# Kernel tuning notes

Measured on AMD Instinct MI355X. Metric: run time of the kernel, lower is better.

The kernel has to match this reference:

```python
import jax, jax.numpy as jnp
import numpy as np

N_NODES = 100000
N_EDGES = 1600000
D_IN = 128
D_HID = 128
D_OUT = 10
N_GRAPHS = 512


def setup_inputs() -> dict:
    key = jax.random.key(0)
    ks = jax.random.split(key, 12)
    x = jax.random.normal(ks[0], (N_NODES, D_IN), dtype=jnp.float32)
    edge_index = jax.random.randint(ks[1], (2, N_EDGES), 0, N_NODES, dtype=jnp.int64)
    batch = jnp.sort(jax.random.randint(ks[2], (N_NODES,), 0, N_GRAPHS, dtype=jnp.int64))
    s = 1.0 / np.sqrt(D_HID)
    W0 = jax.random.normal(ks[3], (D_HID, D_IN), dtype=jnp.float32) * s
    b0 = jax.random.normal(ks[4], (D_HID,), dtype=jnp.float32) * s
    W1 = jax.random.normal(ks[5], (D_HID, D_HID), dtype=jnp.float32) * s
    b1 = jax.random.normal(ks[6], (D_HID,), dtype=jnp.float32) * s
    W2 = jax.random.normal(ks[7], (D_HID, D_HID), dtype=jnp.float32) * s
    b2 = jax.random.normal(ks[8], (D_HID,), dtype=jnp.float32) * s
    Wg = jax.random.normal(ks[9], (D_OUT, D_HID), dtype=jnp.float32) * s
    bg = jax.random.normal(ks[10], (D_OUT,), dtype=jnp.float32) * s
    return {"x": x, "edge_index": edge_index, "batch": batch,
            "W0": W0, "b0": b0, "W1": W1, "b1": b1, "W2": W2, "b2": b2,
            "Wg": Wg, "bg": bg}


def _gin_conv(x, src, dst, W, b):
    # GINConv with eps=0: Linear(x + sum_{j in N(i)} x_j)
    agg = jax.ops.segment_sum(x[src], dst, num_segments=N_NODES)  # [N, d]
    return (x + agg) @ W.T + b


def reference(x, edge_index, batch, W0, b0, W1, b1, W2, b2, Wg, bg):
    src, dst = edge_index[0], edge_index[1]
    h = jax.nn.relu(_gin_conv(x, src, dst, W0, b0))
    h = jax.nn.relu(_gin_conv(h, src, dst, W1, b1))
    h = _gin_conv(h, src, dst, W2, b2)
    # global_mean_pool over graph ids
    sums = jax.ops.segment_sum(h, batch, num_segments=N_GRAPHS)            # [G, d]
    counts = jax.ops.segment_sum(jnp.ones((N_NODES,), h.dtype), batch, num_segments=N_GRAPHS)
    pooled = sums / jnp.maximum(counts, 1.0)[:, None]                       # [G, d]
    return pooled @ Wg.T + bg                                               # [G, out]
```

## Files before the change

### kernel.cpp

```cpp
#include <hip/hip_runtime.h>

#define N_NODES 100000
#define N_EDGES 1600000
#define N_GRAPHS 512
#define NBUCK 391
#define EPB 2048
#define NB_SCAT ((N_EDGES + EPB - 1) / EPB)
#define CAPB 4864
#define CONV_BLKS 6250

typedef _Float16 half8 __attribute__((ext_vector_type(8)));
typedef float floatx4 __attribute__((ext_vector_type(4)));

union U16 { uint4 u; half8 h; };

__global__ __launch_bounds__(256) void convert_pack(const float4* __restrict__ X4,
                                                    uint4* __restrict__ Xh,
                                                    const float* __restrict__ W0,
                                                    const float* __restrict__ W1,
                                                    const float* __restrict__ W2,
                                                    uint4* __restrict__ Bp,
                                                    int* __restrict__ gcur) {
    int bid = blockIdx.x, tid = threadIdx.x;
    if (bid < CONV_BLKS) {
        int t = bid * 256 + tid;
        float4 a = X4[t * 2], b = X4[t * 2 + 1];
        U16 o;
        o.h[0] = (_Float16)a.x; o.h[1] = (_Float16)a.y;
        o.h[2] = (_Float16)a.z; o.h[3] = (_Float16)a.w;
        o.h[4] = (_Float16)b.x; o.h[5] = (_Float16)b.y;
        o.h[6] = (_Float16)b.z; o.h[7] = (_Float16)b.w;
        Xh[t] = o.u;
    } else {
        int zi = (bid - CONV_BLKS) * 256 + tid;
        if (zi < NBUCK) gcur[zi] = 0;
        int slice = (bid - CONV_BLKS) * 4 + (tid >> 6);
        if (slice >= 96) return;
        int l = tid & 63;
        int layer = slice >> 5;
        int r = slice & 31;
        int c = r >> 3, f = r & 7;
        const float* W = (layer == 0) ? W0 : (layer == 1) ? W1 : W2;
        int col = f * 16 + (l & 15);
        int k0 = c * 32 + (l >> 4) * 8;
        U16 o;
        #pragma unroll
        for (int j = 0; j < 8; ++j) o.h[j] = (_Float16)W[col * 128 + k0 + j];
        Bp[layer * 2048 + (c * 8 + f) * 64 + l] = o.u;
    }
}

__global__ __launch_bounds__(256) void bucket_scatter(const int* __restrict__ src,
                                                      const int* __restrict__ dst,
                                                      int* __restrict__ gcur,
                                                      unsigned* __restrict__ pairs) {
    __shared__ int cnt[NBUCK];
    __shared__ int base[NBUCK];
    int tid = threadIdx.x;
    for (int i = tid; i < NBUCK; i += 256) cnt[i] = 0;
    __syncthreads();
    int e0 = blockIdx.x * EPB, e1 = min(e0 + EPB, N_EDGES);
    for (int e = e0 + tid; e < e1; e += 256) atomicAdd(&cnt[dst[e] >> 8], 1);
    __syncthreads();
    for (int i = tid; i < NBUCK; i += 256) {
        int v = cnt[i];
        base[i] = i * CAPB + (v ? atomicAdd(&gcur[i], v) : 0);
        cnt[i] = 0;
    }
    __syncthreads();
    for (int e = e0 + tid; e < e1; e += 256) {
        int d = dst[e], b = d >> 8;
        int r = atomicAdd(&cnt[b], 1);
        pairs[base[b] + r] = (unsigned)src[e] | ((unsigned)(d & 255) << 17);
    }
}

__global__ __launch_bounds__(256) void bucket_fine(const unsigned* __restrict__ pairs,
                                                   const int* __restrict__ gcur,
                                                   int* __restrict__ off,
                                                   int* __restrict__ srclist) {
    __shared__ int snap[NBUCK];
    __shared__ int ncnt[256];
    __shared__ int ws[4];
    int tid = threadIdx.x, b = blockIdx.x;
    int lane = tid & 63, w = tid >> 6;

    for (int i = tid; i < NBUCK; i += 256) snap[i] = gcur[i];
    ncnt[tid] = 0;
    __syncthreads();
    if (tid < 64) {
        int carry = 0;
        for (int base = 0; base < NBUCK; base += 64) {
            int i = base + tid;
            int v = (i < NBUCK) ? snap[i] : 0;
            int incl = v;
            #pragma unroll
            for (int s = 1; s < 64; s <<= 1) {
                int y = __shfl_up(incl, s, 64);
                if (tid >= s) incl += y;
            }
            if (i < NBUCK) snap[i] = carry + incl - v;
            carry += __shfl(incl, 63, 64);
        }
    }
    __syncthreads();
    int eLo = snap[b];
    int eNext = (b == NBUCK - 1) ? N_EDGES : snap[b + 1];
    int m = eNext - eLo;
    int sb = b * CAPB;
    if (b == 0 && tid == 0) off[N_NODES] = N_EDGES;
    __syncthreads();

    for (int t = tid; t < m; t += 256) {
        unsigned p = pairs[sb + t];
        atomicAdd(&ncnt[(p >> 17) & 255], 1);
    }
    __syncthreads();
    int v = ncnt[tid];
    int incl = v;
    #pragma unroll
    for (int s = 1; s < 64; s <<= 1) { int y = __shfl_up(incl, s, 64); if (lane >= s) incl += y; }
    if (lane == 63) ws[w] = incl;
    __syncthreads();
    if (tid < 4) {
        int t = ws[tid];
        #pragma unroll
        for (int s = 1; s < 4; s <<= 1) { int y = __shfl_up(t, s, 64); if (tid >= s) t += y; }
        ws[tid] = t;
    }
    __syncthreads();
    int excl = (w ? ws[w - 1] : 0) + incl - v;
    int n = (b << 8) + tid;
    if (n < N_NODES) off[n] = eLo + excl;
    __syncthreads();
    ncnt[tid] = excl;
    __syncthreads();
    for (int t = tid; t < m; t += 256) {
        unsigned p = pairs[sb + t];
        int r = atomicAdd(&ncnt[(p >> 17) & 255], 1);
        srclist[eLo + r] = (int)(p & 0x1FFFFu);
    }
}

__global__ __launch_bounds__(256) void gin_fused(const uint4* __restrict__ Xh,
                                                 const uint4* __restrict__ Bp,
                                                 const float* __restrict__ bias,
                                                 _Float16* __restrict__ H,
                                                 const int* __restrict__ off,
                                                 const int* __restrict__ srclist,
                                                 int doRelu) {
    __shared__ ushort lds[16 * 136];
    int tid = threadIdx.x;
    int n0 = blockIdx.x * 16;
    int r = tid >> 4;
    int c = tid & 15;
    int n = n0 + r;

    int j0 = off[n], j1 = off[n + 1];
    U16 acc; acc.u = Xh[(size_t)n * 16 + c];
    half8 a = acc.h;
    int j = j0;
    for (; j + 3 < j1; j += 4) {
        int s0 = srclist[j], s1 = srclist[j + 1], s2 = srclist[j + 2], s3 = srclist[j + 3];
        U16 v0, v1, v2, v3;
        v0.u = Xh[(size_t)s0 * 16 + c];
        v1.u = Xh[(size_t)s1 * 16 + c];
        v2.u = Xh[(size_t)s2 * 16 + c];
        v3.u = Xh[(size_t)s3 * 16 + c];
        a += v0.h; a += v1.h; a += v2.h; a += v3.h;
    }
    for (; j < j1; ++j) {
        U16 v; v.u = Xh[(size_t)srclist[j] * 16 + c];
        a += v.h;
    }
    U16 o; o.h = a;
    *(uint4*)&lds[r * 136 + c * 8] = o.u;
    __syncthreads();

    int wid = tid >> 6, lane = tid & 63;
    int lrow = lane & 15;
    int lk8 = (lane >> 4) * 8;

    floatx4 acc2[2];
    acc2[0] = (floatx4)0.f;
    acc2[1] = (floatx4)0.f;
    #pragma unroll
    for (int c4 = 0; c4 < 4; ++c4) {
        U16 af; af.u = *(const uint4*)&lds[lrow * 136 + c4 * 32 + lk8];
        #pragma unroll
        for (int q = 0; q < 2; ++q) {
            int f = wid * 2 + q;
            U16 b; b.u = Bp[(c4 * 8 + f) * 64 + lane];
            acc2[q] = __builtin_amdgcn_mfma_f32_16x16x32_f16(b.h, af.h, acc2[q], 0, 0, 0);
        }
    }

    int ncol = lane & 15;
    int rq = (lane >> 4) * 4;
    int node = n0 + ncol;
    #pragma unroll
    for (int q = 0; q < 2; ++q) {
        int f = wid * 2 + q;
        float4 bv = *(const float4*)(bias + f * 16 + rq);
        float o0 = acc2[q][0] + bv.x;
        float o1 = acc2[q][1] + bv.y;
        float o2 = acc2[q][2] + bv.z;
        float o3 = acc2[q][3] + bv.w;
        if (doRelu) {
            o0 = fmaxf(o0, 0.f); o1 = fmaxf(o1, 0.f);
            o2 = fmaxf(o2, 0.f); o3 = fmaxf(o3, 0.f);
        }
        ushort4 st;
        st.x = (unsigned short)__builtin_bit_cast(unsigned short, (_Float16)o0);
        st.y = (unsigned short)__builtin_bit_cast(unsigned short, (_Float16)o1);
        st.z = (unsigned short)__builtin_bit_cast(unsigned short, (_Float16)o2);
        st.w = (unsigned short)__builtin_bit_cast(unsigned short, (_Float16)o3);
        *(ushort4*)(H + (size_t)node * 128 + f * 16 + rq) = st;
    }
}

__device__ __forceinline__ int lower_bound_i(const int* a, int n, int val) {
    int lo = 0, hi = n;
    while (lo < hi) {
        int mid = (lo + hi) >> 1;
        if (a[mid] < val) lo = mid + 1; else hi = mid;
    }
    return lo;
}

__global__ __launch_bounds__(256) void pool_kernel(const uint4* __restrict__ Hh,
                                                   const int* __restrict__ batch,
                                                   const float* __restrict__ Wg,
                                                   const float* __restrict__ bg,
                                                   float* __restrict__ out) {
    __shared__ float p[16 * 128];
    __shared__ float pooled[128];
    int g = blockIdx.x, tid = threadIdx.x;
    int c = tid & 15, r = tid >> 4;
    int lo = lower_bound_i(batch, N_NODES, g);
    int hi = lower_bound_i(batch, N_NODES, g + 1);
    float acc[8] = {0, 0, 0, 0, 0, 0, 0, 0};
    for (int i = lo + r; i < hi; i += 16) {
        U16 v; v.u = Hh[(size_t)i * 16 + c];
        #pragma unroll
        for (int k = 0; k < 8; ++k) acc[k] += (float)v.h[k];
    }
    #pragma unroll
    for (int k = 0; k < 8; ++k) p[r * 128 + c * 8 + k] = acc[k];
    __syncthreads();
    if (tid < 128) {
        float s = 0.f;
        #pragma unroll
        for (int q = 0; q < 16; ++q) s += p[q * 128 + tid];
        pooled[tid] = s / fmaxf((float)(hi - lo), 1.0f);
    }
    __syncthreads();
    if (tid < 10) {
        float s = bg[tid];
        #pragma unroll 4
        for (int k = 0; k < 128; ++k) s += pooled[k] * Wg[tid * 128 + k];
        out[g * 10 + tid] = s;
    }
}

extern "C" void kernel_launch(void* const* d_in, const int* in_sizes, int n_in,
                              void* d_out, int out_size, void* d_ws, size_t ws_size,
                              hipStream_t stream) {
    const float* x   = (const float*)d_in[0];
    const int*   ei  = (const int*)d_in[1];
    const int*   bat = (const int*)d_in[2];
    const float* W0  = (const float*)d_in[3];
    const float* b0  = (const float*)d_in[4];
    const float* W1  = (const float*)d_in[5];
    const float* b1  = (const float*)d_in[6];
    const float* W2  = (const float*)d_in[7];
    const float* b2  = (const float*)d_in[8];
    const float* Wg  = (const float*)d_in[9];
    const float* bg  = (const float*)d_in[10];
    float* out = (float*)d_out;

    const int* src = ei;
    const int* dst = ei + N_EDGES;

    char* w = (char*)d_ws;
    unsigned* pairs = (unsigned*)(w);
    _Float16* P0    = (_Float16*)(w + 25600000);
    _Float16* P1    = (_Float16*)(w + 51200000);
    _Float16* P2    = (_Float16*)(w + 76800000);
    int*    srclist = (int*)(w + 102400000);
    int*    off     = (int*)(w + 108800000);
    uint4*  Bp      = (uint4*)(w + 109300000);
    int*    gcur    = (int*)(w + 109450000);

    convert_pack<<<CONV_BLKS + 24, 256, 0, stream>>>((const float4*)x, (uint4*)P0,
                                                     W0, W1, W2, Bp, gcur);
    bucket_scatter<<<NB_SCAT, 256, 0, stream>>>(src, dst, gcur, pairs);
    bucket_fine<<<NBUCK, 256, 0, stream>>>(pairs, gcur, off, srclist);

    int grid = N_NODES / 16;

    gin_fused<<<grid, 256, 0, stream>>>((const uint4*)P0, Bp, b0, P1, off, srclist, 1);
    gin_fused<<<grid, 256, 0, stream>>>((const uint4*)P1, Bp + 2048, b1, P2, off, srclist, 1);
    gin_fused<<<grid, 256, 0, stream>>>((const uint4*)P2, Bp + 4096, b2, P0, off, srclist, 0);

    pool_kernel<<<N_GRAPHS, 256, 0, stream>>>((const uint4*)P0, bat, Wg, bg, out);
}
```

Before: 282.6 us.

## Halve bucket width for edge sorting and process two node tiles per GIN block

The coarse edge bucketing now uses 128-node buckets (782 buckets) instead of 256-node buckets. This doubles the number of bucket_fine blocks, spreading that stage across more CUs, and shrinks the per-bucket scan to 128 entries. The GIN layer kernel now handles 32 nodes per block as two sequential 16-node gather+MFMA phases with separate LDS buffers, which halves the grid size. That fewer-but-longer-block scheme may lose latency hiding on the irregular gathers in exchange for a smaller launch and some amortised setup.

```diff
diff --git a/kernel.cpp b/kernel.cpp
--- a/kernel.cpp
+++ b/kernel.cpp
@@ -3,10 +3,10 @@
 #define N_NODES 100000
 #define N_EDGES 1600000
 #define N_GRAPHS 512
-#define NBUCK 391
+#define NBUCK 782
 #define EPB 2048
 #define NB_SCAT ((N_EDGES + EPB - 1) / EPB)
-#define CAPB 4864
+#define CAPB 2688
 #define CONV_BLKS 6250
 
 typedef _Float16 half8 __attribute__((ext_vector_type(8)));
@@ -60,7 +60,7 @@
     for (int i = tid; i < NBUCK; i += 256) cnt[i] = 0;
     __syncthreads();
     int e0 = blockIdx.x * EPB, e1 = min(e0 + EPB, N_EDGES);
-    for (int e = e0 + tid; e < e1; e += 256) atomicAdd(&cnt[dst[e] >> 8], 1);
+    for (int e = e0 + tid; e < e1; e += 256) atomicAdd(&cnt[dst[e] >> 7], 1);
     __syncthreads();
     for (int i = tid; i < NBUCK; i += 256) {
         int v = cnt[i];
@@ -69,9 +69,9 @@
     }
     __syncthreads();
     for (int e = e0 + tid; e < e1; e += 256) {
-        int d = dst[e], b = d >> 8;
+        int d = dst[e], b = d >> 7;
         int r = atomicAdd(&cnt[b], 1);
-        pairs[base[b] + r] = (unsigned)src[e] | ((unsigned)(d & 255) << 17);
+        pairs[base[b] + r] = (unsigned)src[e] | ((unsigned)(d & 127) << 17);
     }
 }
 
@@ -80,16 +80,16 @@
                                                    int* __restrict__ off,
                                                    int* __restrict__ srclist) {
     __shared__ int snap[NBUCK];
-    __shared__ int ncnt[256];
-    __shared__ int ws[4];
+    __shared__ int ncnt[128];
+    __shared__ int ws[2];
     int tid = threadIdx.x, b = blockIdx.x;
-    int lane = tid & 63, w = tid >> 6;
 
     for (int i = tid; i < NBUCK; i += 256) snap[i] = gcur[i];
-    ncnt[tid] = 0;
+    if (tid < 128) ncnt[tid] = 0;
     __syncthreads();
     if (tid < 64) {
         int carry = 0;
+        #pragma unroll 1
         for (int base = 0; base < NBUCK; base += 64) {
             int i = base + tid;
             int v = (i < NBUCK) ? snap[i] : 0;
@@ -113,49 +113,40 @@
 
     for (int t = tid; t < m; t += 256) {
         unsigned p = pairs[sb + t];
-        atomicAdd(&ncnt[(p >> 17) & 255], 1);
-    }
-    __syncthreads();
-    int v = ncnt[tid];
-    int incl = v;
-    #pragma unroll
-    for (int s = 1; s < 64; s <<= 1) { int y = __shfl_up(incl, s, 64); if (lane >= s) incl += y; }
-    if (lane == 63) ws[w] = incl;
-    __syncthreads();
-    if (tid < 4) {
-        int t = ws[tid];
-        #pragma unroll
-        for (int s = 1; s < 4; s <<= 1) { int y = __shfl_up(t, s, 64); if (tid >= s) t += y; }
-        ws[tid] = t;
-    }
-    __syncthreads();
-    int excl = (w ? ws[w - 1] : 0) + incl - v;
-    int n = (b << 8) + tid;
-    if (n < N_NODES) off[n] = eLo + excl;
-    __syncthreads();
-    ncnt[tid] = excl;
+        atomicAdd(&ncnt[(p >> 17) & 127], 1);
+    }
+    __syncthreads();
+    int v = 0, incl = 0;
+    if (tid < 128) {
+        v = ncnt[tid];
+        incl = v;
+        int lane = tid & 63;
+        #pragma unroll
+        for (int s = 1; s < 64; s <<= 1) {
+            int y = __shfl_up(incl, s, 64);
+            if (lane >= s) incl += y;
+        }
+        if (lane == 63) ws[tid >> 6] = incl;
+    }
+    __syncthreads();
+    if (tid < 128) {
+        int excl = (tid >= 64 ? ws[0] : 0) + incl - v;
+        int n = (b << 7) + tid;
+        if (n < N_NODES) off[n] = eLo + excl;
+        ncnt[tid] = excl;
+    }
     __syncthreads();
     for (int t = tid; t < m; t += 256) {
         unsigned p = pairs[sb + t];
-        int r = atomicAdd(&ncnt[(p >> 17) & 255], 1);
+        int r = atomicAdd(&ncnt[(p >> 17) & 127], 1);
         srclist[eLo + r] = (int)(p & 0x1FFFFu);
     }
 }
 
-__global__ __launch_bounds__(256) void gin_fused(const uint4* __restrict__ Xh,
-                                                 const uint4* __restrict__ Bp,
-                                                 const float* __restrict__ bias,
-                                                 _Float16* __restrict__ H,
-                                                 const int* __restrict__ off,
-                                                 const int* __restrict__ srclist,
-                                                 int doRelu) {
-    __shared__ ushort lds[16 * 136];
-    int tid = threadIdx.x;
-    int n0 = blockIdx.x * 16;
-    int r = tid >> 4;
-    int c = tid & 15;
-    int n = n0 + r;
-
+__device__ __forceinline__ half8 gather_row(const uint4* __restrict__ Xh,
+                                            const int* __restrict__ off,
+                                            const int* __restrict__ srclist,
+                                            int n, int c) {
     int j0 = off[n], j1 = off[n + 1];
     U16 acc; acc.u = Xh[(size_t)n * 16 + c];
     half8 a = acc.h;
@@ -173,20 +164,22 @@
         U16 v; v.u = Xh[(size_t)srclist[j] * 16 + c];
         a += v.h;
     }
-    U16 o; o.h = a;
-    *(uint4*)&lds[r * 136 + c * 8] = o.u;
-    __syncthreads();
-
-    int wid = tid >> 6, lane = tid & 63;
+    return a;
+}
+
+__device__ __forceinline__ void mfma_store(const ushort* __restrict__ buf,
+                                           const uint4* __restrict__ Bp,
+                                           const float* __restrict__ bias,
+                                           _Float16* __restrict__ H,
+                                           int nodebase, int wid, int lane, int doRelu) {
     int lrow = lane & 15;
     int lk8 = (lane >> 4) * 8;
-
     floatx4 acc2[2];
     acc2[0] = (floatx4)0.f;
     acc2[1] = (floatx4)0.f;
     #pragma unroll
     for (int c4 = 0; c4 < 4; ++c4) {
-        U16 af; af.u = *(const uint4*)&lds[lrow * 136 + c4 * 32 + lk8];
+        U16 af; af.u = *(const uint4*)&buf[lrow * 136 + c4 * 32 + lk8];
         #pragma unroll
         for (int q = 0; q < 2; ++q) {
             int f = wid * 2 + q;
@@ -194,10 +187,9 @@
             acc2[q] = __builtin_amdgcn_mfma_f32_16x16x32_f16(b.h, af.h, acc2[q], 0, 0, 0);
         }
     }
-
     int ncol = lane & 15;
     int rq = (lane >> 4) * 4;
-    int node = n0 + ncol;
+    int node = nodebase + ncol;
     #pragma unroll
     for (int q = 0; q < 2; ++q) {
         int f = wid * 2 + q;
@@ -219,6 +211,35 @@
     }
 }
 
+__global__ __launch_bounds__(256) void gin_fused(const uint4* __restrict__ Xh,
+                                                 const uint4* __restrict__ Bp,
+                                                 const float* __restrict__ bias,
+                                                 _Float16* __restrict__ H,
+                                                 const int* __restrict__ off,
+                                                 const int* __restrict__ srclist,
+                                                 int doRelu) {
+    __shared__ ushort lds[2][16 * 136];
+    int tid = threadIdx.x;
+    int n0 = blockIdx.x * 32;
+    int r = tid >> 4, c = tid & 15;
+    int wid = tid >> 6, lane = tid & 63;
+
+    {
+        half8 a = gather_row(Xh, off, srclist, n0 + r, c);
+        U16 o; o.h = a;
+        *(uint4*)&lds[0][r * 136 + c * 8] = o.u;
+    }
+    __syncthreads();
+    mfma_store(lds[0], Bp, bias, H, n0, wid, lane, doRelu);
+    {
+        half8 a = gather_row(Xh, off, srclist, n0 + 16 + r, c);
+        U16 o; o.h = a;
+        *(uint4*)&lds[1][r * 136 + c * 8] = o.u;
+    }
+    __syncthreads();
+    mfma_store(lds[1], Bp, bias, H, n0 + 16, wid, lane, doRelu);
+}
+
 __device__ __forceinline__ int lower_bound_i(const int* a, int n, int val) {
     int lo = 0, hi = n;
     while (lo < hi) {
@@ -297,7 +318,7 @@
     bucket_scatter<<<NB_SCAT, 256, 0, stream>>>(src, dst, gcur, pairs);
     bucket_fine<<<NBUCK, 256, 0, stream>>>(pairs, gcur, off, srclist);
 
-    int grid = N_NODES / 16;
+    int grid = N_NODES / 32;
 
     gin_fused<<<grid, 256, 0, stream>>>((const uint4*)P0, Bp, b0, P1, off, srclist, 1);
     gin_fused<<<grid, 256, 0, stream>>>((const uint4*)P1, Bp + 2048, b1, P2, off, srclist, 1);
```

Result: slower. 300.7 us (+6.4%).
